# Performance work log

Hardware: AMD Instinct MI355X
Metric: run time of the kernel (lower is better)

The kernel has to match this reference:

```python
import jax, jax.numpy as jnp
import numpy as np

N, E, D, A = 50000, 1_600_000, 32, 2
H1, C1, H2, C2 = 4, 16, 2, 32  # GATv2Conv(D,16,heads=4) -> 64; GATv2Conv(64,32,heads=2) -> 64


def setup_inputs() -> dict:
    key = jax.random.key(0)
    ks = jax.random.split(key, 16)

    def glorot(k, shape):
        fan = shape[0] + shape[-1]
        return jax.random.normal(k, shape, jnp.float32) * np.float32(np.sqrt(2.0 / fan))

    return {
        "x": jax.random.normal(ks[0], (N, D), jnp.float32),
        "edge_index": jax.random.randint(ks[1], (2, E), 0, N),
        "edge_attr": jax.random.normal(ks[2], (E, 2), jnp.float32),
        # GATv2 layer 1 (lin_l/lin_r with bias, lin_edge no bias, att [H,C], out bias)
        "w1_l": glorot(ks[3], (D, H1 * C1)), "b1_l": jnp.zeros((H1 * C1,), jnp.float32),
        "w1_r": glorot(ks[4], (D, H1 * C1)), "b1_r": jnp.zeros((H1 * C1,), jnp.float32),
        "w1_e": glorot(ks[5], (2, H1 * C1)),
        "att1": glorot(ks[6], (H1, C1)),
        "bias1": jnp.zeros((H1 * C1,), jnp.float32),
        # GATv2 layer 2
        "w2_l": glorot(ks[7], (H1 * C1, H2 * C2)), "b2_l": jnp.zeros((H2 * C2,), jnp.float32),
        "w2_r": glorot(ks[8], (H1 * C1, H2 * C2)), "b2_r": jnp.zeros((H2 * C2,), jnp.float32),
        "w2_e": glorot(ks[9], (2, H2 * C2)),
        "att2": glorot(ks[10], (H2, C2)),
        "bias2": jnp.zeros((H2 * C2,), jnp.float32),
        # heads
        "w_actor": glorot(ks[11], (H2 * C2, A)), "b_actor": jnp.zeros((A,), jnp.float32),
        "w_critic": glorot(ks[12], (H2 * C2, 1)), "b_critic": jnp.zeros((1,), jnp.float32),
        "log_std": jnp.zeros((A,), jnp.float32),
    }


def _gatv2(x, src, dst, eattr, Wl, bl, Wr, br, We, att, bias, H, C, n):
    # PyG GATv2Conv: message j->i with i = dst, j = src
    xl = (x @ Wl + bl).reshape(n, H, C)  # source-side transform (x_j)
    xr = (x @ Wr + br).reshape(n, H, C)  # target-side transform (x_i)
    ee = (eattr @ We).reshape(-1, H, C)  # per-edge embedding
    z = jax.nn.leaky_relu(xl[src] + xr[dst] + ee, 0.2)  # [Etot, H, C]
    logits = jnp.einsum('ehc,hc->eh', z, att)  # [Etot, H]
    # segment softmax over incoming edges of each dst node
    m = jax.ops.segment_max(logits, dst, num_segments=n)
    p = jnp.exp(logits - m[dst])
    denom = jax.ops.segment_sum(p, dst, num_segments=n)
    alpha = p / denom[dst]  # every node has a self-loop -> denom > 0
    msg = xl[src] * alpha[:, :, None]  # [Etot, H, C]
    out = jax.ops.segment_sum(msg, dst, num_segments=n)
    return out.reshape(n, H * C) + bias


def reference(x, edge_index, edge_attr,
              w1_l, b1_l, w1_r, b1_r, w1_e, att1, bias1,
              w2_l, b2_l, w2_r, b2_r, w2_e, att2, bias2,
              w_actor, b_actor, w_critic, b_critic, log_std):
    src, dst = edge_index[0], edge_index[1]
    # add_self_loops=True, fill_value='mean': self-loop edge_attr = mean of incoming edge_attr
    cnt = jax.ops.segment_sum(jnp.ones((edge_attr.shape[0],), x.dtype), dst, num_segments=N)
    sums = jax.ops.segment_sum(edge_attr, dst, num_segments=N)
    loop_attr = sums / jnp.maximum(cnt, 1.0)[:, None]
    loop = jnp.arange(N, dtype=src.dtype)
    src_f = jnp.concatenate([src, loop])
    dst_f = jnp.concatenate([dst, loop])
    ea = jnp.concatenate([edge_attr, loop_attr], axis=0)

    h = jax.nn.relu(_gatv2(x, src_f, dst_f, ea, w1_l, b1_l, w1_r, b1_r, w1_e, att1, bias1, H1, C1, N))
    h = jax.nn.relu(_gatv2(h, src_f, dst_f, ea, w2_l, b2_l, w2_r, b2_r, w2_e, att2, bias2, H2, C2, N))

    action_mean = jnp.tanh(h @ w_actor + b_actor)  # [N, A]
    value = h @ w_critic + b_critic               # [N, 1]
    std = jnp.exp(log_std)                        # [A]  (Normal(action_mean, std))
    return action_mean, std, value
```

## Files before the change

### kernel.cpp

```cpp
#include <hip/hip_runtime.h>
#include <hip/hip_fp16.h>
#include <math.h>

#define DIN   32
#define F1    64
#define F2    64

typedef __attribute__((ext_vector_type(2))) float f32x2;

__device__ __forceinline__ f32x2 pkfma(f32x2 a, f32x2 b, f32x2 c) {
#if __has_builtin(__builtin_elementwise_fma)
    return __builtin_elementwise_fma(a, b, c);
#else
    return a * b + c;
#endif
}
__device__ __forceinline__ f32x2 pkmax(f32x2 a, f32x2 b) {
    f32x2 r; r.x = fmaxf(a.x, b.x); r.y = fmaxf(a.y, b.y); return r;
}

__device__ __forceinline__ unsigned bf16pack(float a, float b) {
    unsigned ua = __float_as_uint(a);
    unsigned ub = __float_as_uint(b);
    ua = (ua + 0x7FFFu + ((ua >> 16) & 1u)) >> 16;
    ub = (ub + 0x7FFFu + ((ub >> 16) & 1u)) >> 16;
    return ua | (ub << 16);
}

template <int K>
__device__ __forceinline__ void lin_lr_body(int bid,
        const float* __restrict__ x,
        const float* __restrict__ Wl, const float* __restrict__ bl,
        const float* __restrict__ Wr, const float* __restrict__ br,
        __half* __restrict__ xl, float* __restrict__ xr, int n) {
    __shared__ float Ash[32][K + 4];
    __shared__ float Wsh[K][128];
    const int t = threadIdx.x;
    const int node0 = bid * 32;

    for (int idx = t; idx < 32 * (K / 4); idx += 256) {
        int m = idx / (K / 4), kq = idx % (K / 4);
        float4 v = make_float4(0.f, 0.f, 0.f, 0.f);
        if (node0 + m < n) v = ((const float4*)(x + (size_t)(node0 + m) * K))[kq];
        *(float4*)&Ash[m][kq * 4] = v;
    }
    for (int idx = t; idx < K * 32; idx += 256) {
        int k = idx / 32, j4 = idx % 32;
        float4 v = (j4 < 16) ? ((const float4*)(Wl + (size_t)k * 64))[j4]
                             : ((const float4*)(Wr + (size_t)k * 64))[j4 - 16];
        *(float4*)&Wsh[k][j4 * 4] = v;
    }
    __syncthreads();

    const int ty = t >> 4;
    const int tx = t & 15;
    f32x2 c0[4], c1[4];
#pragma unroll
    for (int j = 0; j < 4; j++) {
        c0[j].x = 0.f; c0[j].y = 0.f;
        c1[j].x = 0.f; c1[j].y = 0.f;
    }

#pragma unroll 4
    for (int k = 0; k < K; k++) {
        float a0 = Ash[ty * 2 + 0][k];
        float a1 = Ash[ty * 2 + 1][k];
        float4 w0 = *(const float4*)&Wsh[k][tx * 8];
        float4 w1 = *(const float4*)&Wsh[k][tx * 8 + 4];
        f32x2 wv0; wv0.x = w0.x; wv0.y = w0.y;
        f32x2 wv1; wv1.x = w0.z; wv1.y = w0.w;
        f32x2 wv2; wv2.x = w1.x; wv2.y = w1.y;
        f32x2 wv3; wv3.x = w1.z; wv3.y = w1.w;
        f32x2 a0s; a0s.x = a0; a0s.y = a0;
        f32x2 a1s; a1s.x = a1; a1s.y = a1;
        c0[0] = pkfma(a0s, wv0, c0[0]);
        c0[1] = pkfma(a0s, wv1, c0[1]);
        c0[2] = pkfma(a0s, wv2, c0[2]);
        c0[3] = pkfma(a0s, wv3, c0[3]);
        c1[0] = pkfma(a1s, wv0, c1[0]);
        c1[1] = pkfma(a1s, wv1, c1[1]);
        c1[2] = pkfma(a1s, wv2, c1[2]);
        c1[3] = pkfma(a1s, wv3, c1[3]);
    }

    const float* bsrc = (tx < 8) ? bl : br;
    int jb = (tx < 8) ? tx * 8 : (tx - 8) * 8;
    float4 b0 = ((const float4*)(bsrc + jb))[0];
    float4 b1 = ((const float4*)(bsrc + jb))[1];
#pragma unroll
    for (int m = 0; m < 2; m++) {
        int node = node0 + ty * 2 + m;
        if (node >= n) continue;
        const f32x2* cc = (m == 0) ? c0 : c1;
        float o0 = cc[0].x + b0.x, o1 = cc[0].y + b0.y;
        float o2 = cc[1].x + b0.z, o3 = cc[1].y + b0.w;
        float o4 = cc[2].x + b1.x, o5 = cc[2].y + b1.y;
        float o6 = cc[3].x + b1.z, o7 = cc[3].y + b1.w;
        if (tx < 8) {
            __half2 h0 = __floats2half2_rn(o0, o1);
            __half2 h1 = __floats2half2_rn(o2, o3);
            __half2 h2 = __floats2half2_rn(o4, o5);
            __half2 h3 = __floats2half2_rn(o6, o7);
            uint4 pk;
            pk.x = *(unsigned*)&h0; pk.y = *(unsigned*)&h1;
            pk.z = *(unsigned*)&h2; pk.w = *(unsigned*)&h3;
            *((uint4*)(xl + (size_t)node * 64 + jb)) = pk;
        } else {
            float4 f0 = make_float4(o0, o1, o2, o3);
            float4 f1 = make_float4(o4, o5, o6, o7);
            ((float4*)(xr + (size_t)node * 64 + jb))[0] = f0;
            ((float4*)(xr + (size_t)node * 64 + jb))[1] = f1;
        }
    }
}

__global__ __launch_bounds__(256, 2)
void fused_scatter_lin1(const int* __restrict__ srcr, const int* __restrict__ dstr,
                        const float* __restrict__ ea, int* __restrict__ cursor,
                        int2* __restrict__ inter,
                        int E, int Ec, int NB, int cap, int gridCnt,
                        const float* __restrict__ x,
                        const float* __restrict__ Wl, const float* __restrict__ bl,
                        const float* __restrict__ Wr, const float* __restrict__ br,
                        __half* __restrict__ xl, float* __restrict__ xr, int n) {
    if ((int)blockIdx.x >= gridCnt) {
        lin_lr_body<DIN>(blockIdx.x - gridCnt, x, Wl, bl, Wr, br, xl, xr, n);
        return;
    }
    __shared__ int hist[256];
    __shared__ int colsh[256];
    __shared__ unsigned short rksh[3584];
    const int blk = blockIdx.x;
    const int t = threadIdx.x;
    hist[t] = 0;
    __syncthreads();
    const int s0 = blk * Ec, s1 = min(E, s0 + Ec);
    for (int e = s0 + t; e < s1; e += 256)
        rksh[e - s0] = (unsigned short)atomicAdd(&hist[dstr[e] >> 8], 1);
    __syncthreads();
    if (t < NB) {
        int h = hist[t];
        int off = h ? atomicAdd(&cursor[t], h) : 0;
        colsh[t] = t * cap + off;
    }
    __syncthreads();
    for (int e = s0 + t; e < s1; e += 256) {
        int d = dstr[e];
        float2 v = ((const float2*)ea)[e];
        int2 r;
        r.x = srcr[e] | ((d & 255) << 24);
        r.y = (int)bf16pack(v.x, v.y);
        inter[colsh[d >> 8] + (int)rksh[e - s0]] = r;
    }
}

__global__ __launch_bounds__(512)
void bucket_csr(const int2* __restrict__ inter, const int* __restrict__ cursor,
                int2* __restrict__ rse, int2* __restrict__ edges,
                int NB, int N, int cap) {
    __shared__ int sh[256];
    __shared__ int cur[256];
    const int b = blockIdx.x, t = threadIdx.x;
    const int bstart = b * cap;
    const int bend = bstart + cursor[b];

    if (t < 256) sh[t] = 0;
    __syncthreads();
    for (int pos = bstart + t; pos < bend; pos += 512)
        atomicAdd(&sh[((unsigned)inter[pos].x) >> 24], 1);
    __syncthreads();
    int cnt_v = 0;
    if (t < 256) cnt_v = sh[t];
    __syncthreads();
    if (t < 256) sh[t] = cnt_v;
    __syncthreads();
    for (int off = 1; off < 256; off <<= 1) {
        int x = (t >= off && t < 256) ? sh[t - off] : 0;
        __syncthreads();
        if (t < 256) sh[t] += x;
        __syncthreads();
    }
    if (t < 256) {
        int excl = sh[t] - cnt_v;
        cur[t] = excl;
        int myrs = bstart + excl;
        int node = b * 256 + t;
        if (node < N) rse[node] = make_int2(myrs, myrs + cnt_v);
    }
    __syncthreads();
    for (int pos = bstart + t; pos < bend; pos += 512) {
        int2 r = inter[pos];
        int k = atomicAdd(&cur[((unsigned)r.x) >> 24], 1);
        r.x &= 0x00FFFFFF;
        edges[bstart + k] = r;
    }
    int zend = (b + 1) * cap + ((b == NB - 1) ? 64 : 0);
    for (int pos = bend + t; pos < zend; pos += 512)
        edges[pos] = make_int2(0, 0);
}

__global__ __launch_bounds__(256, 2)
void lin_lr_tiled64(const float* __restrict__ x,
                    const float* __restrict__ Wl, const float* __restrict__ bl,
                    const float* __restrict__ Wr, const float* __restrict__ br,
                    __half* __restrict__ xl, float* __restrict__ xr, int n) {
    lin_lr_body<F1>(blockIdx.x, x, Wl, bl, Wr, br, xl, xr, n);
}

template <int H, int C, bool FUSE_HEADS>
__global__ __launch_bounds__(256)
void gat_kernel(const __half* __restrict__ xl, const float* __restrict__ xr,
                const int2* __restrict__ rse,
                const int2* __restrict__ edges,
                const float* __restrict__ We, const float* __restrict__ att,
                const float* __restrict__ bias, float* __restrict__ hout,
                const float* __restrict__ wa, const float* __restrict__ ba,
                const float* __restrict__ wc, const float* __restrict__ bc,
                const float* __restrict__ ls, float* __restrict__ pout,
                int n) {
    constexpr int LPH = C / 4;
    if (FUSE_HEADS && blockIdx.x == 0 && threadIdx.x < 2)
        pout[(size_t)n * 2 + threadIdx.x] = expf(ls[threadIdx.x]);
    const int lane = threadIdx.x & 63;
    const int wid = (blockIdx.x * blockDim.x + threadIdx.x) >> 6;
    if (wid >= n) return;
    const int i = wid;
    const int g = lane >> 4;
    const int q = lane & 15;

    const uint2* xlh = (const uint2*)xl;
    const float4 xri4 = ((const float4*)(xr + (size_t)i * 64))[q];
    const float4 we04 = ((const float4*)We)[q];
    const float4 we14 = ((const float4*)(We + 64))[q];
    const float4 av4 = ((const float4*)att)[q];
    const float LOG2E = 1.4426950408889634f;
    f32x2 xrlo; xrlo.x = xri4.x; xrlo.y = xri4.y;
    f32x2 xrhi; xrhi.x = xri4.z; xrhi.y = xri4.w;
    f32x2 we0lo; we0lo.x = we04.x; we0lo.y = we04.y;
    f32x2 we0hi; we0hi.x = we04.z; we0hi.y = we04.w;
    f32x2 we1lo; we1lo.x = we14.x; we1lo.y = we14.y;
    f32x2 we1hi; we1hi.x = we14.z; we1hi.y = we14.w;
    f32x2 avlo; avlo.x = av4.x * LOG2E; avlo.y = av4.y * LOG2E;
    f32x2 avhi; avhi.x = av4.z * LOG2E; avhi.y = av4.w * LOG2E;

    auto h4lo = [](uint2 h) -> f32x2 {
        float2 a = __half22float2(*(__half2*)&h.x);
        f32x2 r; r.x = a.x; r.y = a.y; return r;
    };
    auto h4hi = [](uint2 h) -> f32x2 {
        float2 b = __half22float2(*(__half2*)&h.y);
        f32x2 r; r.x = b.x; r.y = b.y; return r;
    };
    auto logit_of = [&](f32x2 xlo, f32x2 xhi, float ea0, float ea1) -> float {
        f32x2 e0; e0.x = ea0; e0.y = ea0;
        f32x2 e1; e1.x = ea1; e1.y = ea1;
        f32x2 ylo = xlo + pkfma(e0, we0lo, pkfma(e1, we1lo, xrlo));
        f32x2 yhi = xhi + pkfma(e0, we0hi, pkfma(e1, we1hi, xrhi));
        ylo = pkmax(ylo, ylo * 0.2f);
        yhi = pkmax(yhi, yhi * 0.2f);
        f32x2 l2 = pkfma(ylo, avlo, yhi * avhi);
        return l2.x + l2.y;
    };

    float den = 0.f;
    float sea0 = 0.f, sea1 = 0.f;
    f32x2 aclo; aclo.x = 0.f; aclo.y = 0.f;
    f32x2 achi; achi.x = 0.f; achi.y = 0.f;

    const int2 se = rse[i];
    const int e0 = se.x, e1 = se.y;
    const int r = (e1 - e0) & 7;

    if (r) {
        int2 h0 = edges[e0 + g];
        int2 h1 = edges[e0 + 4 + g];
        uint2 u0 = xlh[(h0.x << 4) + q];
        uint2 u1 = xlh[(h1.x << 4) + q];
        f32x2 x0lo = h4lo(u0), x0hi = h4hi(u0);
        f32x2 x1lo = h4lo(u1), x1hi = h4hi(u1);
        const bool v0 = g < r;
        const bool v1 = (4 + g) < r;
        float ea00 = v0 ? __int_as_float(h0.y << 16) : 0.f;
        float ea01 = v0 ? __int_as_float(h0.y & 0xFFFF0000) : 0.f;
        float ea10 = v1 ? __int_as_float(h1.y << 16) : 0.f;
        float ea11 = v1 ? __int_as_float(h1.y & 0xFFFF0000) : 0.f;
        sea0 += ea00 + ea10;
        sea1 += ea01 + ea11;
        float l0 = logit_of(x0lo, x0hi, ea00, ea01);
        float l1 = logit_of(x1lo, x1hi, ea10, ea11);
#pragma unroll
        for (int m = 1; m < LPH; m <<= 1) {
            l0 += __shfl_xor(l0, m, 64);
            l1 += __shfl_xor(l1, m, 64);
        }
        float p0 = v0 ? exp2f(l0) : 0.f;
        float p1 = v1 ? exp2f(l1) : 0.f;
        den += p0 + p1;
        f32x2 p0s; p0s.x = p0; p0s.y = p0;
        f32x2 p1s; p1s.x = p1; p1s.y = p1;
        aclo = pkfma(p0s, x0lo, pkfma(p1s, x1lo, aclo));
        achi = pkfma(p0s, x0hi, pkfma(p1s, x1hi, achi));
    }

    const int em = e0 + r;
    int2 rn0 = edges[em + g];
    int2 rn1 = edges[em + 4 + g];
    uint2 xpn0 = xlh[(rn0.x << 4) + q];
    uint2 xpn1 = xlh[(rn1.x << 4) + q];

    for (int eb = em; eb < e1; eb += 8) {
        int2 r0 = rn0, r1 = rn1;
        f32x2 x0lo = h4lo(xpn0), x0hi = h4hi(xpn0);
        f32x2 x1lo = h4lo(xpn1), x1hi = h4hi(xpn1);
        rn0 = edges[eb + 8 + g];
        rn1 = edges[eb + 12 + g];
        xpn0 = xlh[(rn0.x << 4) + q];
        xpn1 = xlh[(rn1.x << 4) + q];

        float ea00 = __int_as_float(r0.y << 16);
        float ea01 = __int_as_float(r0.y & 0xFFFF0000);
        float ea10 = __int_as_float(r1.y << 16);
        float ea11 = __int_as_float(r1.y & 0xFFFF0000);
        sea0 += ea00 + ea10;
        sea1 += ea01 + ea11;

        float l0 = logit_of(x0lo, x0hi, ea00, ea01);
        float l1 = logit_of(x1lo, x1hi, ea10, ea11);
#pragma unroll
        for (int m = 1; m < LPH; m <<= 1) {
            l0 += __shfl_xor(l0, m, 64);
            l1 += __shfl_xor(l1, m, 64);
        }
        float p0 = exp2f(l0);
        float p1 = exp2f(l1);
        den += p0 + p1;
        f32x2 p0s; p0s.x = p0; p0s.y = p0;
        f32x2 p1s; p1s.x = p1; p1s.y = p1;
        aclo = pkfma(p0s, x0lo, pkfma(p1s, x1lo, aclo));
        achi = pkfma(p0s, x0hi, pkfma(p1s, x1hi, achi));
    }

    float a0 = aclo.x, a1 = aclo.y, a2 = achi.x, a3 = achi.y;

#pragma unroll
    for (int m = 16; m < 64; m <<= 1) {
        den += __shfl_xor(den, m, 64);
        a0 += __shfl_xor(a0, m, 64);
        a1 += __shfl_xor(a1, m, 64);
        a2 += __shfl_xor(a2, m, 64);
        a3 += __shfl_xor(a3, m, 64);
        sea0 += __shfl_xor(sea0, m, 64);
        sea1 += __shfl_xor(sea1, m, 64);
    }

    const int cnt_i = e1 - e0;
    const float invc = cnt_i ? 1.0f / (float)cnt_i : 0.f;
    const float lamx = sea0 * invc;
    const float lamy = sea1 * invc;
    uint2 us = xlh[(i << 4) + q];
    f32x2 xslo = h4lo(us), xshi = h4hi(us);
    {
        float l = logit_of(xslo, xshi, lamx, lamy);
#pragma unroll
        for (int m = 1; m < LPH; m <<= 1) l += __shfl_xor(l, m, 64);
        float p = exp2f(l);
        den += p;
        a0 = fmaf(p, xslo.x, a0);
        a1 = fmaf(p, xslo.y, a1);
        a2 = fmaf(p, xshi.x, a2);
        a3 = fmaf(p, xshi.y, a3);
    }

    float rd = 1.0f / den;
    const float4 bv = ((const float4*)bias)[q];
    float4 o;
    o.x = fmaxf(fmaf(a0, rd, bv.x), 0.f);
    o.y = fmaxf(fmaf(a1, rd, bv.y), 0.f);
    o.z = fmaxf(fmaf(a2, rd, bv.z), 0.f);
    o.w = fmaxf(fmaf(a3, rd, bv.w), 0.f);

    if (!FUSE_HEADS) {
        if (g == 0) ((float4*)(hout + (size_t)i * 64))[q] = o;
    } else {
        float4 wa01 = ((const float4*)wa)[q * 2];
        float4 wa23 = ((const float4*)wa)[q * 2 + 1];
        float4 wcv  = ((const float4*)wc)[q];
        float d0 = o.x * wa01.x + o.y * wa01.z + o.z * wa23.x + o.w * wa23.z;
        float d1 = o.x * wa01.y + o.y * wa01.w + o.z * wa23.y + o.w * wa23.w;
        float d2 = o.x * wcv.x + o.y * wcv.y + o.z * wcv.z + o.w * wcv.w;
#pragma unroll
        for (int m = 1; m < 16; m <<= 1) {
            d0 += __shfl_xor(d0, m, 64);
            d1 += __shfl_xor(d1, m, 64);
            d2 += __shfl_xor(d2, m, 64);
        }
        if (lane == 0) {
            pout[(size_t)i * 2 + 0] = tanhf(d0 + ba[0]);
            pout[(size_t)i * 2 + 1] = tanhf(d1 + ba[1]);
            pout[(size_t)n * 2 + 2 + i] = d2 + bc[0];
        }
    }
}


extern "C" void kernel_launch(void* const* d_in, const int* in_sizes, int n_in,
                              void* d_out, int out_size, void* d_ws, size_t ws_size,
                              hipStream_t stream) {
    const float* x    = (const float*)d_in[0];
    const int*   ei   = (const int*)  d_in[1];
    const float* ea   = (const float*)d_in[2];
    const float* w1l  = (const float*)d_in[3];
    const float* b1l  = (const float*)d_in[4];
    const float* w1r  = (const float*)d_in[5];
    const float* b1r  = (const float*)d_in[6];
    const float* w1e  = (const float*)d_in[7];
    const float* att1 = (const float*)d_in[8];
    const float* bias1= (const float*)d_in[9];
    const float* w2l  = (const float*)d_in[10];
    const float* b2l  = (const float*)d_in[11];
    const float* w2r  = (const float*)d_in[12];
    const float* b2r  = (const float*)d_in[13];
    const float* w2e  = (const float*)d_in[14];
    const float* att2 = (const float*)d_in[15];
    const float* bias2= (const float*)d_in[16];
    const float* wa   = (const float*)d_in[17];
    const float* ba   = (const float*)d_in[18];
    const float* wc   = (const float*)d_in[19];
    const float* bc   = (const float*)d_in[20];
    const float* ls   = (const float*)d_in[21];

    const int N = in_sizes[0] / DIN;
    const int E = in_sizes[2] / 2;
    const int* srcr = ei;
    const int* dstr = ei + E;

    const int NB = (N + 255) >> 8;
    const int NCH = 512;
    const int Ec = (E + NCH - 1) / NCH;
    int cap = (E + NB - 1) / NB;
    cap = ((cap + cap / 4) + 63) & ~63;

    char* p = (char*)d_ws;
    auto alloc = [&](size_t bytes) -> void* {
        void* r = (void*)p;
        p += (bytes + 255) & ~(size_t)255;
        return r;
    };
    int*    cursor = (int*)   alloc(256 * 4);
    int2*   rse    = (int2*)  alloc((size_t)N * 8);
    int2*   edges  = (int2*)  alloc(((size_t)NB * cap + 64) * 8);
    __half* xl     = (__half*)alloc((size_t)N * F1 * 2);
    float*  xr     = (float*) alloc((size_t)N * F1 * 4);
    float*  h1     = (float*) alloc((size_t)N * F1 * 4);
    float*  h2     = (float*) alloc((size_t)N * F2 * 4);
    int2* inter = (int2*)h1;
    (void)ws_size; (void)n_in; (void)out_size;

    hipMemsetAsync(cursor, 0, 256 * 4, stream);

    const int TB = 256;
    int gridGemm = (N + 31) / 32;
    int gridWave = (N + 3) / 4;

    fused_scatter_lin1<<<NCH + gridGemm, TB, 0, stream>>>(
        srcr, dstr, ea, cursor, inter, E, Ec, NB, cap, NCH,
        x, w1l, b1l, w1r, b1r, xl, xr, N);
    bucket_csr<<<NB, 512, 0, stream>>>(inter, cursor, rse, edges, NB, N, cap);

    gat_kernel<4, 16, false><<<gridWave, TB, 0, stream>>>(
        xl, xr, rse, edges, w1e, att1, bias1, h1,
        nullptr, nullptr, nullptr, nullptr, nullptr, nullptr, N);
    lin_lr_tiled64<<<gridGemm, TB, 0, stream>>>(h1, w2l, b2l, w2r, b2r, xl, xr, N);
    gat_kernel<2, 32, true><<<gridWave, TB, 0, stream>>>(
        xl, xr, rse, edges, w2e, att2, bias2, h2,
        wa, ba, wc, bc, ls, (float*)d_out, N);
}
```

Measured before the change: 294.5 us.

## Stage edge records in LDS for scatter and fuse layer-1 linear into CSR build

The bucket-scatter kernel becomes a 512-thread count_scatter that reads src, dst and edge_attr once, keeping packed records, bucket ids and ranks in shared memory so the second pass no longer re-reads global inputs. The layer-1 linear transform moves out of the scatter kernel and is fused with the per-bucket CSR build, now run with 256 threads per block, so the GEMM blocks overlap with the CSR work instead of the scatter. This trades higher LDS use per scatter block (lower occupancy) and a narrower CSR block for fewer global reads.

Measured after the change: 284.1 us. 1.04x faster.

```diff
diff --git a/kernel.cpp b/kernel.cpp
--- a/kernel.cpp
+++ b/kernel.cpp
@@ -114,73 +114,77 @@
     }
 }
 
-__global__ __launch_bounds__(256, 2)
-void fused_scatter_lin1(const int* __restrict__ srcr, const int* __restrict__ dstr,
-                        const float* __restrict__ ea, int* __restrict__ cursor,
-                        int2* __restrict__ inter,
-                        int E, int Ec, int NB, int cap, int gridCnt,
-                        const float* __restrict__ x,
-                        const float* __restrict__ Wl, const float* __restrict__ bl,
-                        const float* __restrict__ Wr, const float* __restrict__ br,
-                        __half* __restrict__ xl, float* __restrict__ xr, int n) {
-    if ((int)blockIdx.x >= gridCnt) {
-        lin_lr_body<DIN>(blockIdx.x - gridCnt, x, Wl, bl, Wr, br, xl, xr, n);
-        return;
-    }
+__global__ __launch_bounds__(512, 2)
+void count_scatter(const int* __restrict__ srcr, const int* __restrict__ dstr,
+                   const float* __restrict__ ea, int* __restrict__ cursor,
+                   int2* __restrict__ inter, int E, int Ec, int NB, int cap) {
+    __shared__ int2 recsh[3584];
+    __shared__ unsigned short rksh[3584];
+    __shared__ unsigned char bksh[3584];
     __shared__ int hist[256];
     __shared__ int colsh[256];
-    __shared__ unsigned short rksh[3584];
     const int blk = blockIdx.x;
     const int t = threadIdx.x;
-    hist[t] = 0;
+    if (t < 256) hist[t] = 0;
     __syncthreads();
     const int s0 = blk * Ec, s1 = min(E, s0 + Ec);
-    for (int e = s0 + t; e < s1; e += 256)
-        rksh[e - s0] = (unsigned short)atomicAdd(&hist[dstr[e] >> 8], 1);
-    __syncthreads();
-    if (t < NB) {
-        int h = hist[t];
-        int off = h ? atomicAdd(&cursor[t], h) : 0;
-        colsh[t] = t * cap + off;
-    }
-    __syncthreads();
-    for (int e = s0 + t; e < s1; e += 256) {
+    const int cnt = s1 - s0;
+    for (int e = s0 + t; e < s1; e += 512) {
         int d = dstr[e];
         float2 v = ((const float2*)ea)[e];
         int2 r;
         r.x = srcr[e] | ((d & 255) << 24);
         r.y = (int)bf16pack(v.x, v.y);
-        inter[colsh[d >> 8] + (int)rksh[e - s0]] = r;
-    }
-}
-
-__global__ __launch_bounds__(512)
-void bucket_csr(const int2* __restrict__ inter, const int* __restrict__ cursor,
-                int2* __restrict__ rse, int2* __restrict__ edges,
-                int NB, int N, int cap) {
+        int li = e - s0;
+        int bk = (unsigned)d >> 8;
+        recsh[li] = r;
+        bksh[li] = (unsigned char)bk;
+        rksh[li] = (unsigned short)atomicAdd(&hist[bk], 1);
+    }
+    __syncthreads();
+    if (t < NB) {
+        int h = hist[t];
+        colsh[t] = t * cap + (h ? atomicAdd(&cursor[t], h) : 0);
+    }
+    __syncthreads();
+    for (int li = t; li < cnt; li += 512)
+        inter[colsh[bksh[li]] + (int)rksh[li]] = recsh[li];
+}
+
+__global__ __launch_bounds__(256, 2)
+void fused_csr_lin1(const int2* __restrict__ inter, const int* __restrict__ cursor,
+                    int2* __restrict__ rse, int2* __restrict__ edges,
+                    int NB, int N, int cap,
+                    const float* __restrict__ x,
+                    const float* __restrict__ Wl, const float* __restrict__ bl,
+                    const float* __restrict__ Wr, const float* __restrict__ br,
+                    __half* __restrict__ xl, float* __restrict__ xr, int n) {
+    if ((int)blockIdx.x >= NB) {
+        lin_lr_body<DIN>(blockIdx.x - NB, x, Wl, bl, Wr, br, xl, xr, n);
+        return;
+    }
     __shared__ int sh[256];
     __shared__ int cur[256];
     const int b = blockIdx.x, t = threadIdx.x;
     const int bstart = b * cap;
     const int bend = bstart + cursor[b];
 
-    if (t < 256) sh[t] = 0;
-    __syncthreads();
-    for (int pos = bstart + t; pos < bend; pos += 512)
+    sh[t] = 0;
+    __syncthreads();
+    for (int pos = bstart + t; pos < bend; pos += 256)
         atomicAdd(&sh[((unsigned)inter[pos].x) >> 24], 1);
     __syncthreads();
-    int cnt_v = 0;
-    if (t < 256) cnt_v = sh[t];
-    __syncthreads();
-    if (t < 256) sh[t] = cnt_v;
+    int cnt_v = sh[t];
+    __syncthreads();
+    sh[t] = cnt_v;
     __syncthreads();
     for (int off = 1; off < 256; off <<= 1) {
-        int x = (t >= off && t < 256) ? sh[t - off] : 0;
+        int xv = (t >= off) ? sh[t - off] : 0;
         __syncthreads();
-        if (t < 256) sh[t] += x;
+        sh[t] += xv;
         __syncthreads();
     }
-    if (t < 256) {
+    {
         int excl = sh[t] - cnt_v;
         cur[t] = excl;
         int myrs = bstart + excl;
@@ -188,14 +192,14 @@
         if (node < N) rse[node] = make_int2(myrs, myrs + cnt_v);
     }
     __syncthreads();
-    for (int pos = bstart + t; pos < bend; pos += 512) {
+    for (int pos = bstart + t; pos < bend; pos += 256) {
         int2 r = inter[pos];
         int k = atomicAdd(&cur[((unsigned)r.x) >> 24], 1);
         r.x &= 0x00FFFFFF;
         edges[bstart + k] = r;
     }
     int zend = (b + 1) * cap + ((b == NB - 1) ? 64 : 0);
-    for (int pos = bend + t; pos < zend; pos += 512)
+    for (int pos = bend + t; pos < zend; pos += 256)
         edges[pos] = make_int2(0, 0);
 }
 
@@ -462,10 +466,11 @@
     int gridGemm = (N + 31) / 32;
     int gridWave = (N + 3) / 4;
 
-    fused_scatter_lin1<<<NCH + gridGemm, TB, 0, stream>>>(
-        srcr, dstr, ea, cursor, inter, E, Ec, NB, cap, NCH,
+    count_scatter<<<NCH, 512, 0, stream>>>(srcr, dstr, ea, cursor, inter,
+                                           E, Ec, NB, cap);
+    fused_csr_lin1<<<NB + gridGemm, TB, 0, stream>>>(
+        inter, cursor, rse, edges, NB, N, cap,
         x, w1l, b1l, w1r, b1r, xl, xr, N);
-    bucket_csr<<<NB, 512, 0, stream>>>(inter, cursor, rse, edges, NB, N, cap);
 
     gat_kernel<4, 16, false><<<gridWave, TB, 0, stream>>>(
         xl, xr, rse, edges, w1e, att1, bias1, h1,
```
